# Kernel optimization log

Hardware: AMD Instinct MI355X
Metric: run time of the kernel (lower is better)

Reference implementation:

```python
import jax, jax.numpy as jnp
import numpy as np
import math

# --- delta-LFIT rule-space combinatorics ---
NUM_VARS, DELAYS = 3, 3
N = NUM_VARS * DELAYS  # 9 delayed variables

def delta_count(l, n):
    # number of rule bodies of length exactly l: choose l of n vars, each with a polarity
    return math.comb(n, l) * (2 ** l)

MAX_RULE_LEN = max(delta_count(l, N) for l in range(N + 1))  # 5376
OUT_DIM = MAX_RULE_LEN + 1  # padded logits + trailing 'empty rule' logit
N_HEADS = N + 1  # rules_pred has heads for rule_len = 0..N

B, S = 512, 1
DIM_IN = 1024
DIM_HIDDEN = 1024
LAYERS = 4  # -> LAYERS+1 Linear layers total (no nonlinearity in the original Sequential)


def setup_inputs() -> dict:
    key = jax.random.key(0)
    ks = jax.random.split(key, 4)
    latent = jax.random.normal(ks[0], (B, S, DIM_IN), dtype=jnp.float32)
    rule_len = jax.random.randint(ks[1], (B,), 0, N_HEADS, dtype=jnp.int32)

    n_lin = LAYERS + 1  # dim_in==dim_hidden so all trunk linears stack uniformly
    scale = 1.0 / np.sqrt(DIM_HIDDEN)
    W_mlp = jax.random.normal(ks[2], (n_lin, DIM_HIDDEN, DIM_HIDDEN), dtype=jnp.float32) * scale
    b_mlp = jnp.zeros((n_lin, DIM_HIDDEN), dtype=jnp.float32)

    # Padded head weight bank: row layout matches torch.cat((out[..., :-1], zeros_pad, out[..., -1:]))
    rng = np.random.default_rng(0)
    Wh = np.zeros((N_HEADS, OUT_DIM, DIM_HIDDEN), dtype=np.float32)
    bh = np.zeros((N_HEADS, OUT_DIM), dtype=np.float32)
    for l in range(N_HEADS):
        d = delta_count(l, N) + 1  # head l output dim: length(l)-length(l-1)+1
        w = (rng.standard_normal((d, DIM_HIDDEN)) * scale).astype(np.float32)
        b = (rng.standard_normal(d) * 0.01).astype(np.float32)
        Wh[l, : d - 1] = w[:-1]
        Wh[l, OUT_DIM - 1] = w[-1]
        bh[l, : d - 1] = b[:-1]
        bh[l, OUT_DIM - 1] = b[-1]

    return {
        "latent": latent,
        "W_mlp": W_mlp,
        "b_mlp": b_mlp,
        "W_heads": jnp.asarray(Wh),
        "b_heads": jnp.asarray(bh),
        "rule_len": rule_len,
    }


def reference(latent, W_mlp, b_mlp, W_heads, b_heads, rule_len):
    # Trunk: stack of Linear layers, no activation (matches the original Sequential)
    h = latent  # [B, S, H]
    for i in range(W_mlp.shape[0]):
        h = h @ W_mlp[i].T + b_mlp[i]
    # Per-sample dynamic head dispatch (rule_len_is_diff=True branch), vectorized:
    # compute all padded heads, then gather each sample's head.
    all_out = jnp.einsum('bsh,loh->bslo', h, W_heads) + b_heads  # [B, S, N_HEADS, OUT_DIM]
    idx = rule_len.astype(jnp.int32)[:, None, None, None]  # [B,1,1,1]
    out = jnp.take_along_axis(all_out, idx, axis=2)[:, :, 0, :]  # [B, S, OUT_DIM]
    return out
```

## Files before the change

kernel.cpp:

```cpp
#include <hip/hip_runtime.h>

#define DIM     1024
#define BATCH   512
#define OUTD    5377
#define NHEADS  10
#define NLAYERS 5
#define LDK     72

typedef __attribute__((ext_vector_type(4))) float f32x4;
typedef __attribute__((ext_vector_type(8))) short bf16x8;

__device__ __forceinline__ unsigned short f2bf(float f) {
    unsigned u = __builtin_bit_cast(unsigned, f);
    u = (u + 0x7FFFu + ((u >> 16) & 1u)) >> 16;
    return (unsigned short)u;
}
__device__ __forceinline__ float bf2f(unsigned short h) {
    unsigned u = ((unsigned)h) << 16;
    return __builtin_bit_cast(float, u);
}

__global__ void group_kernel(const int* __restrict__ rule_len,
                             int* __restrict__ bidx,
                             int* __restrict__ gstart,
                             int* __restrict__ gcount) {
    __shared__ int s_count[NHEADS];
    __shared__ int s_fill[NHEADS];
    int t = threadIdx.x;
    if (t < NHEADS) s_count[t] = 0;
    __syncthreads();
    int h = rule_len[t];
    atomicAdd(&s_count[h], 1);
    __syncthreads();
    if (t == 0) {
        int acc = 0;
        for (int i = 0; i < NHEADS; ++i) {
            gstart[i] = acc;
            gcount[i] = s_count[i];
            s_fill[i] = acc;
            acc += s_count[i];
        }
    }
    __syncthreads();
    int pos = atomicAdd(&s_fill[h], 1);
    bidx[pos] = t;
}

__global__ void convert_latent(const float* __restrict__ in,
                               unsigned short* __restrict__ out) {
    int i = blockIdx.x * blockDim.x + threadIdx.x;
    float4 v = ((const float4*)in)[i];
    ushort4 o;
    o.x = f2bf(v.x); o.y = f2bf(v.y); o.z = f2bf(v.z); o.w = f2bf(v.w);
    ((ushort4*)out)[i] = o;
}

__global__ __launch_bounds__(256) void mlp_mfma(
    const unsigned short* __restrict__ A,
    const float* __restrict__ W,
    const float* __restrict__ bias,
    unsigned short* __restrict__ C)
{
    __shared__ __align__(16) unsigned short As[2][32][LDK];
    __shared__ __align__(16) unsigned short Whi[2][32][LDK];
    __shared__ __align__(16) unsigned short Wlo[2][32][LDK];

    const int tid = threadIdx.x;
    const int n0 = blockIdx.x * 32;
    const int m0 = blockIdx.y * 32;
    const int lane = tid & 63;
    const int wid = tid >> 6;
    const int wm = (wid >> 1) * 16;
    const int wn = (wid & 1) * 16;

    f32x4 acc = {0.f, 0.f, 0.f, 0.f};

    const int ar = tid >> 3;
    const int ac = (tid & 7) * 8;
    const int wr = tid >> 4;
    const int wc = (tid & 15) * 4;

    const unsigned short* Ap = A + (size_t)(m0 + ar) * DIM + ac;
    const float* Wp0 = W + (size_t)(n0 + wr) * DIM + wc;
    const float* Wp1 = W + (size_t)(n0 + wr + 16) * DIM + wc;

    uint4  ra  = *(const uint4*)(Ap);
    float4 rw0 = *(const float4*)(Wp0);
    float4 rw1 = *(const float4*)(Wp1);

    for (int t = 0; t < DIM / 64; ++t) {
        const int cur = t & 1;
        *(uint4*)&As[cur][ar][ac] = ra;
        {
            ushort4 hi, lo;
            hi.x = f2bf(rw0.x); lo.x = f2bf(rw0.x - bf2f(hi.x));
            hi.y = f2bf(rw0.y); lo.y = f2bf(rw0.y - bf2f(hi.y));
            hi.z = f2bf(rw0.z); lo.z = f2bf(rw0.z - bf2f(hi.z));
            hi.w = f2bf(rw0.w); lo.w = f2bf(rw0.w - bf2f(hi.w));
            *(ushort4*)&Whi[cur][wr][wc] = hi;
            *(ushort4*)&Wlo[cur][wr][wc] = lo;
            hi.x = f2bf(rw1.x); lo.x = f2bf(rw1.x - bf2f(hi.x));
            hi.y = f2bf(rw1.y); lo.y = f2bf(rw1.y - bf2f(hi.y));
            hi.z = f2bf(rw1.z); lo.z = f2bf(rw1.z - bf2f(hi.z));
            hi.w = f2bf(rw1.w); lo.w = f2bf(rw1.w - bf2f(hi.w));
            *(ushort4*)&Whi[cur][wr + 16][wc] = hi;
            *(ushort4*)&Wlo[cur][wr + 16][wc] = lo;
        }
        __syncthreads();
        if (t < DIM / 64 - 1) {
            const int k0 = (t + 1) * 64;
            ra  = *(const uint4*)(Ap + k0);
            rw0 = *(const float4*)(Wp0 + k0);
            rw1 = *(const float4*)(Wp1 + k0);
        }
        #pragma unroll
        for (int kk = 0; kk < 2; ++kk) {
            const int ko = kk * 32 + (lane >> 4) * 8;
            bf16x8 a  = *(const bf16x8*)&As[cur][wm + (lane & 15)][ko];
            bf16x8 bh = *(const bf16x8*)&Whi[cur][wn + (lane & 15)][ko];
            bf16x8 bl = *(const bf16x8*)&Wlo[cur][wn + (lane & 15)][ko];
            acc = __builtin_amdgcn_mfma_f32_16x16x32_bf16(a, bh, acc, 0, 0, 0);
            acc = __builtin_amdgcn_mfma_f32_16x16x32_bf16(a, bl, acc, 0, 0, 0);
        }
    }

    const int cn = n0 + wn + (lane & 15);
    const float bn = bias[cn];
    const int rbase = m0 + wm + (lane >> 4) * 4;
    #pragma unroll
    for (int j = 0; j < 4; ++j) {
        C[(size_t)(rbase + j) * DIM + cn] = f2bf(acc[j] + bn);
    }
}

__global__ __launch_bounds__(256) void head_mfma(
    const unsigned short* __restrict__ H,
    const float* __restrict__ Wh,
    const float* __restrict__ bh,
    const int* __restrict__ bidx,
    const int* __restrict__ gstart,
    const int* __restrict__ gcount,
    float* __restrict__ out)
{
    const int head = blockIdx.z;
    const int cnt = gcount[head];
    const int m0 = blockIdx.y * 64;
    if (m0 >= cnt) return;
    const int n0 = blockIdx.x * 64;

    __shared__ __align__(16) unsigned short As[2][64][LDK];
    __shared__ __align__(16) unsigned short Ws[2][64][LDK];
    __shared__ int s_b[64];

    const int tid = threadIdx.x;
    if (tid < 64) {
        int mi = m0 + tid;
        s_b[tid] = (mi < cnt) ? bidx[gstart[head] + mi] : -1;
    }
    __syncthreads();

    const int lane = tid & 63;
    const int wid = tid >> 6;
    const int wm = (wid >> 1) * 32;
    const int wn = (wid & 1) * 32;

    f32x4 acc[2][2] = {};

    const int ar = tid >> 3;
    const int ac = (tid & 7) * 8;
    int b0 = s_b[ar];       if (b0 < 0) b0 = 0;
    int b1 = s_b[ar + 32];  if (b1 < 0) b1 = 0;
    const unsigned short* Ap0 = H + (size_t)b0 * DIM + ac;
    const unsigned short* Ap1 = H + (size_t)b1 * DIM + ac;

    const int wr = tid >> 4;
    const int wc = (tid & 15) * 4;
    const float* WhL = Wh + (size_t)head * OUTD * DIM;
    const float* Wp[4];
    #pragma unroll
    for (int p = 0; p < 4; ++p) {
        int r = n0 + wr + p * 16;
        if (r > OUTD - 1) r = OUTD - 1;
        Wp[p] = WhL + (size_t)r * DIM + wc;
    }

    uint4 ra0 = *(const uint4*)(Ap0);
    uint4 ra1 = *(const uint4*)(Ap1);
    float4 rw[4];
    #pragma unroll
    for (int p = 0; p < 4; ++p) rw[p] = *(const float4*)(Wp[p]);

    for (int t = 0; t < DIM / 64; ++t) {
        const int cur = t & 1;
        *(uint4*)&As[cur][ar][ac]      = ra0;
        *(uint4*)&As[cur][ar + 32][ac] = ra1;
        #pragma unroll
        for (int p = 0; p < 4; ++p) {
            ushort4 hi;
            hi.x = f2bf(rw[p].x);
            hi.y = f2bf(rw[p].y);
            hi.z = f2bf(rw[p].z);
            hi.w = f2bf(rw[p].w);
            *(ushort4*)&Ws[cur][wr + p * 16][wc] = hi;
        }
        __syncthreads();
        if (t < DIM / 64 - 1) {
            const int k0 = (t + 1) * 64;
            ra0 = *(const uint4*)(Ap0 + k0);
            ra1 = *(const uint4*)(Ap1 + k0);
            #pragma unroll
            for (int p = 0; p < 4; ++p) rw[p] = *(const float4*)(Wp[p] + k0);
        }
        #pragma unroll
        for (int kk = 0; kk < 2; ++kk) {
            const int ko = kk * 32 + (lane >> 4) * 8;
            bf16x8 a0 = *(const bf16x8*)&As[cur][wm + (lane & 15)][ko];
            bf16x8 a1 = *(const bf16x8*)&As[cur][wm + 16 + (lane & 15)][ko];
            bf16x8 w0 = *(const bf16x8*)&Ws[cur][wn + (lane & 15)][ko];
            bf16x8 w1 = *(const bf16x8*)&Ws[cur][wn + 16 + (lane & 15)][ko];
            acc[0][0] = __builtin_amdgcn_mfma_f32_16x16x32_bf16(a0, w0, acc[0][0], 0, 0, 0);
            acc[0][1] = __builtin_amdgcn_mfma_f32_16x16x32_bf16(a0, w1, acc[0][1], 0, 0, 0);
            acc[1][0] = __builtin_amdgcn_mfma_f32_16x16x32_bf16(a1, w0, acc[1][0], 0, 0, 0);
            acc[1][1] = __builtin_amdgcn_mfma_f32_16x16x32_bf16(a1, w1, acc[1][1], 0, 0, 0);
        }
    }

    const float* bhL = bh + (size_t)head * OUTD;
    #pragma unroll
    for (int fm = 0; fm < 2; ++fm) {
        #pragma unroll
        for (int fn = 0; fn < 2; ++fn) {
            int n = n0 + wn + fn * 16 + (lane & 15);
            if (n >= OUTD) continue;
            float bn = bhL[n];
            #pragma unroll
            for (int j = 0; j < 4; ++j) {
                int mi = wm + fm * 16 + (lane >> 4) * 4 + j;
                int b = s_b[mi];
                if (b >= 0) out[(size_t)b * OUTD + n] = acc[fm][fn][j] + bn;
            }
        }
    }
}

extern "C" void kernel_launch(void* const* d_in, const int* in_sizes, int n_in,
                              void* d_out, int out_size, void* d_ws, size_t ws_size,
                              hipStream_t stream) {
    const float* latent   = (const float*)d_in[0];
    const float* W_mlp    = (const float*)d_in[1];
    const float* b_mlp    = (const float*)d_in[2];
    const float* W_heads  = (const float*)d_in[3];
    const float* b_heads  = (const float*)d_in[4];
    const int*   rule_len = (const int*)d_in[5];
    float* out = (float*)d_out;

    unsigned short* h0 = (unsigned short*)d_ws;
    unsigned short* h1 = h0 + (size_t)BATCH * DIM;
    int* bidx   = (int*)(h1 + (size_t)BATCH * DIM);
    int* gstart = bidx + BATCH;
    int* gcount = gstart + 16;

    group_kernel<<<1, BATCH, 0, stream>>>(rule_len, bidx, gstart, gcount);
    convert_latent<<<(BATCH * DIM / 4) / 256, 256, 0, stream>>>(latent, h0);

    dim3 mgrid(DIM / 32, BATCH / 32);
    const unsigned short* src = h0;
    unsigned short* dst = h1;
    for (int l = 0; l < NLAYERS; ++l) {
        mlp_mfma<<<mgrid, 256, 0, stream>>>(src,
                                            W_mlp + (size_t)l * DIM * DIM,
                                            b_mlp + (size_t)l * DIM,
                                            dst);
        const unsigned short* t = src;
        src = dst;
        dst = (unsigned short*)t;
    }

    dim3 hgrid((OUTD + 63) / 64, BATCH / 64, NHEADS);
    head_mfma<<<hgrid, 256, 0, stream>>>(src, W_heads, b_heads,
                                         bidx, gstart, gcount, out);
}
```

Baseline: 123.0 us.

## Narrow head tile to 32 columns and deepen global prefetch to two stages

The head GEMM tile shrinks from 64x64 to 64x32 output columns, doubling the grid and adding an occupancy hint in launch bounds. Global loads are now prefetched two K-steps ahead with register double buffering, and a manual lgkmcnt wait plus raw barrier with sched_barrier replaces __syncthreads. The aim is to hide more latency on the memory-bound fp32 head weight stream. The cost is lower MFMA reuse per block, since the A tile is reloaded twice as often, and more register pressure.

```diff
diff --git a/kernel.cpp b/kernel.cpp
--- a/kernel.cpp
+++ b/kernel.cpp
@@ -18,6 +18,9 @@
 __device__ __forceinline__ float bf2f(unsigned short h) {
     unsigned u = ((unsigned)h) << 16;
     return __builtin_bit_cast(float, u);
+}
+__device__ __forceinline__ unsigned pk2(float a, float b) {
+    return (unsigned)f2bf(a) | ((unsigned)f2bf(b) << 16);
 }
 
 __global__ void group_kernel(const int* __restrict__ rule_len,
@@ -133,7 +136,7 @@
     }
 }
 
-__global__ __launch_bounds__(256) void head_mfma(
+__global__ __launch_bounds__(256, 5) void head_mfma(
     const unsigned short* __restrict__ H,
     const float* __restrict__ Wh,
     const float* __restrict__ bh,
@@ -146,10 +149,10 @@
     const int cnt = gcount[head];
     const int m0 = blockIdx.y * 64;
     if (m0 >= cnt) return;
-    const int n0 = blockIdx.x * 64;
+    const int n0 = blockIdx.x * 32;
 
     __shared__ __align__(16) unsigned short As[2][64][LDK];
-    __shared__ __align__(16) unsigned short Ws[2][64][LDK];
+    __shared__ __align__(16) unsigned short Ws[2][32][LDK];
     __shared__ int s_b[64];
 
     const int tid = threadIdx.x;
@@ -162,9 +165,9 @@
     const int lane = tid & 63;
     const int wid = tid >> 6;
     const int wm = (wid >> 1) * 32;
-    const int wn = (wid & 1) * 32;
-
-    f32x4 acc[2][2] = {};
+    const int wn = (wid & 1) * 16;
+
+    f32x4 acc[2] = {};
 
     const int ar = tid >> 3;
     const int ac = (tid & 7) * 8;
@@ -173,43 +176,43 @@
     const unsigned short* Ap0 = H + (size_t)b0 * DIM + ac;
     const unsigned short* Ap1 = H + (size_t)b1 * DIM + ac;
 
-    const int wr = tid >> 4;
-    const int wc = (tid & 15) * 4;
-    const float* WhL = Wh + (size_t)head * OUTD * DIM;
-    const float* Wp[4];
+    const int wr = tid >> 3;
+    const int wc = (tid & 7) * 8;
+    int wrow = n0 + wr; if (wrow > OUTD - 1) wrow = OUTD - 1;
+    const float* Wp = Wh + (size_t)head * OUTD * DIM + (size_t)wrow * DIM + wc;
+
+    uint4  pa0[2], pa1[2];
+    float4 pw0[2], pw1[2];
+
+    pa0[0] = *(const uint4*)(Ap0);
+    pa1[0] = *(const uint4*)(Ap1);
+    pw0[0] = *(const float4*)(Wp);
+    pw1[0] = *(const float4*)(Wp + 4);
+    pa0[1] = *(const uint4*)(Ap0 + 64);
+    pa1[1] = *(const uint4*)(Ap1 + 64);
+    pw0[1] = *(const float4*)(Wp + 64);
+    pw1[1] = *(const float4*)(Wp + 68);
+
     #pragma unroll
-    for (int p = 0; p < 4; ++p) {
-        int r = n0 + wr + p * 16;
-        if (r > OUTD - 1) r = OUTD - 1;
-        Wp[p] = WhL + (size_t)r * DIM + wc;
-    }
-
-    uint4 ra0 = *(const uint4*)(Ap0);
-    uint4 ra1 = *(const uint4*)(Ap1);
-    float4 rw[4];
-    #pragma unroll
-    for (int p = 0; p < 4; ++p) rw[p] = *(const float4*)(Wp[p]);
-
     for (int t = 0; t < DIM / 64; ++t) {
         const int cur = t & 1;
-        *(uint4*)&As[cur][ar][ac]      = ra0;
-        *(uint4*)&As[cur][ar + 32][ac] = ra1;
-        #pragma unroll
-        for (int p = 0; p < 4; ++p) {
-            ushort4 hi;
-            hi.x = f2bf(rw[p].x);
-            hi.y = f2bf(rw[p].y);
-            hi.z = f2bf(rw[p].z);
-            hi.w = f2bf(rw[p].w);
-            *(ushort4*)&Ws[cur][wr + p * 16][wc] = hi;
-        }
-        __syncthreads();
-        if (t < DIM / 64 - 1) {
-            const int k0 = (t + 1) * 64;
-            ra0 = *(const uint4*)(Ap0 + k0);
-            ra1 = *(const uint4*)(Ap1 + k0);
-            #pragma unroll
-            for (int p = 0; p < 4; ++p) rw[p] = *(const float4*)(Wp[p] + k0);
+        *(uint4*)&As[cur][ar][ac]      = pa0[cur];
+        *(uint4*)&As[cur][ar + 32][ac] = pa1[cur];
+        uint4 wp;
+        wp.x = pk2(pw0[cur].x, pw0[cur].y);
+        wp.y = pk2(pw0[cur].z, pw0[cur].w);
+        wp.z = pk2(pw1[cur].x, pw1[cur].y);
+        wp.w = pk2(pw1[cur].z, pw1[cur].w);
+        *(uint4*)&Ws[cur][wr][wc] = wp;
+        asm volatile("s_waitcnt lgkmcnt(0)" ::: "memory");
+        __builtin_amdgcn_s_barrier();
+        __builtin_amdgcn_sched_barrier(0);
+        if (t + 2 < DIM / 64) {
+            const int k0 = (t + 2) * 64;
+            pa0[cur] = *(const uint4*)(Ap0 + k0);
+            pa1[cur] = *(const uint4*)(Ap1 + k0);
+            pw0[cur] = *(const float4*)(Wp + k0);
+            pw1[cur] = *(const float4*)(Wp + k0 + 4);
         }
         #pragma unroll
         for (int kk = 0; kk < 2; ++kk) {
@@ -217,27 +220,22 @@
             bf16x8 a0 = *(const bf16x8*)&As[cur][wm + (lane & 15)][ko];
             bf16x8 a1 = *(const bf16x8*)&As[cur][wm + 16 + (lane & 15)][ko];
             bf16x8 w0 = *(const bf16x8*)&Ws[cur][wn + (lane & 15)][ko];
-            bf16x8 w1 = *(const bf16x8*)&Ws[cur][wn + 16 + (lane & 15)][ko];
-            acc[0][0] = __builtin_amdgcn_mfma_f32_16x16x32_bf16(a0, w0, acc[0][0], 0, 0, 0);
-            acc[0][1] = __builtin_amdgcn_mfma_f32_16x16x32_bf16(a0, w1, acc[0][1], 0, 0, 0);
-            acc[1][0] = __builtin_amdgcn_mfma_f32_16x16x32_bf16(a1, w0, acc[1][0], 0, 0, 0);
-            acc[1][1] = __builtin_amdgcn_mfma_f32_16x16x32_bf16(a1, w1, acc[1][1], 0, 0, 0);
+            acc[0] = __builtin_amdgcn_mfma_f32_16x16x32_bf16(a0, w0, acc[0], 0, 0, 0);
+            acc[1] = __builtin_amdgcn_mfma_f32_16x16x32_bf16(a1, w0, acc[1], 0, 0, 0);
         }
     }
 
     const float* bhL = bh + (size_t)head * OUTD;
-    #pragma unroll
-    for (int fm = 0; fm < 2; ++fm) {
+    const int n = n0 + wn + (lane & 15);
+    if (n < OUTD) {
+        const float bn = bhL[n];
         #pragma unroll
-        for (int fn = 0; fn < 2; ++fn) {
-            int n = n0 + wn + fn * 16 + (lane & 15);
-            if (n >= OUTD) continue;
-            float bn = bhL[n];
+        for (int fm = 0; fm < 2; ++fm) {
             #pragma unroll
             for (int j = 0; j < 4; ++j) {
                 int mi = wm + fm * 16 + (lane >> 4) * 4 + j;
                 int b = s_b[mi];
-                if (b >= 0) out[(size_t)b * OUTD + n] = acc[fm][fn][j] + bn;
+                if (b >= 0) out[(size_t)b * OUTD + n] = acc[fm][j] + bn;
             }
         }
     }
@@ -271,12 +269,12 @@
                                             W_mlp + (size_t)l * DIM * DIM,
                                             b_mlp + (size_t)l * DIM,
                                             dst);
-        const unsigned short* t = src;
+        unsigned short* t = (unsigned short*)src;
         src = dst;
-        dst = (unsigned short*)t;
-    }
-
-    dim3 hgrid((OUTD + 63) / 64, BATCH / 64, NHEADS);
+        dst = t;
+    }
+
+    dim3 hgrid((OUTD + 31) / 32, BATCH / 64, NHEADS);
     head_mfma<<<hgrid, 256, 0, stream>>>(src, W_heads, b_heads,
                                          bidx, gstart, gcount, out);
 }
```

After: 127.7 us. +3.8%, slower.
